# Optimization experiments

Hardware: AMD Instinct MI355X
Metric: run time of the kernel (lower is better)

The kernel has to match this reference:

```python
import jax, jax.numpy as jnp
import numpy as np

EPS = 1e-12  # torch F.normalize eps

def _normalize(v):
    return v / jnp.maximum(jnp.linalg.norm(v, axis=-1, keepdims=True), EPS)

def setup_inputs() -> dict:
    key = jax.random.key(0)
    ks = jax.random.split(key, 8)
    N, K, D = 500000, 32, 3
    positions = jax.random.normal(ks[0], (N, D), dtype=jnp.float32)
    neighbors = jax.random.normal(ks[1], (N, K, D), dtype=jnp.float32)
    # tiny MLP params: Linear(D,5) -> ReLU -> Linear(5,5) -> ReLU -> Linear(5,1)
    s1 = 1.0 / np.sqrt(D)
    s2 = 1.0 / np.sqrt(5)
    W1 = jax.random.uniform(ks[2], (5, D), jnp.float32, -s1, s1)
    b1 = jax.random.uniform(ks[3], (5,), jnp.float32, -s1, s1)
    W2 = jax.random.uniform(ks[4], (5, 5), jnp.float32, -s2, s2)
    b2 = jax.random.uniform(ks[5], (5,), jnp.float32, -s2, s2)
    W3 = jax.random.uniform(ks[6], (1, 5), jnp.float32, -s2, s2)
    b3 = jax.random.uniform(ks[7], (1,), jnp.float32, -s2, s2)
    return {"positions": positions, "neighbors": neighbors,
            "W1": W1, "b1": b1, "W2": W2, "b2": b2, "W3": W3, "b3": b3}

def reference(positions, neighbors, W1, b1, W2, b2, W3, b3):
    # [N,K,D] normalized neighbor difference vectors
    diffs = neighbors - positions[:, None, :]
    nd = _normalize(diffs)
    # tiny MLP producing a scalar weight per neighbor
    h = jax.nn.relu(jnp.einsum('nkd,hd->nkh', nd, W1) + b1)
    h = jax.nn.relu(jnp.einsum('nkh,gh->nkg', h, W2) + b2)
    w = jnp.einsum('nkh,oh->nko', h, W3) + b3  # [N,K,1]
    vel = jnp.sum(nd * w, axis=1)  # [N,D]
    return _normalize(vel)
```

## Files before the change

### kernel.cpp

```cpp
#include <hip/hip_runtime.h>


#define K 32

__global__ __launch_bounds__(256) void velvec_kernel(
    const float* __restrict__ pos,
    const float* __restrict__ nbr,
    const float* __restrict__ W1,
    const float* __restrict__ b1,
    const float* __restrict__ W2,
    const float* __restrict__ b2,
    const float* __restrict__ W3,
    const float* __restrict__ b3,
    float* __restrict__ out,
    int N)
{
    const int lane  = threadIdx.x & (K - 1);
    const int point = (int)((blockIdx.x * blockDim.x + threadIdx.x) >> 5);
    if (point >= N) return;

    float w1[5][3], bb1[5], w2[5][5], bb2[5], w3[5];
#pragma unroll
    for (int h = 0; h < 5; ++h) {
        bb1[h] = b1[h];
        bb2[h] = b2[h];
        w3[h]  = W3[h];
#pragma unroll
        for (int d = 0; d < 3; ++d) w1[h][d] = W1[h * 3 + d];
#pragma unroll
        for (int g = 0; g < 5; ++g) w2[h][g] = W2[h * 5 + g];
    }
    const float bb3 = b3[0];

    const float px = pos[point * 3 + 0];
    const float py = pos[point * 3 + 1];
    const float pz = pos[point * 3 + 2];

    const float* nb = nbr + (size_t)point * (K * 3) + lane * 3;
    float dx = nb[0] - px;
    float dy = nb[1] - py;
    float dz = nb[2] - pz;
    float n2 = dx * dx + dy * dy + dz * dz;
    float inv = (n2 > 1e-24f) ? __builtin_amdgcn_rsqf(n2) : 1e12f;
    dx *= inv; dy *= inv; dz *= inv;

    float h1[5];
#pragma unroll
    for (int h = 0; h < 5; ++h) {
        float a = bb1[h];
        a = fmaf(w1[h][0], dx, a);
        a = fmaf(w1[h][1], dy, a);
        a = fmaf(w1[h][2], dz, a);
        h1[h] = fmaxf(a, 0.0f);
    }
    float h2[5];
#pragma unroll
    for (int g = 0; g < 5; ++g) {
        float a = bb2[g];
#pragma unroll
        for (int h = 0; h < 5; ++h) a = fmaf(w2[g][h], h1[h], a);
        h2[g] = fmaxf(a, 0.0f);
    }
    float w = bb3;
#pragma unroll
    for (int h = 0; h < 5; ++h) w = fmaf(w3[h], h2[h], w);

    float vx = dx * w, vy = dy * w, vz = dz * w;
#pragma unroll
    for (int m = 16; m > 0; m >>= 1) {
        vx += __shfl_xor(vx, m, K);
        vy += __shfl_xor(vy, m, K);
        vz += __shfl_xor(vz, m, K);
    }

    float vn2  = vx * vx + vy * vy + vz * vz;
    float vinv = (vn2 > 1e-24f) ? __builtin_amdgcn_rsqf(vn2) : 1e12f;
    if (lane < 3) {
        float c = (lane == 0) ? vx : (lane == 1) ? vy : vz;
        out[point * 3 + lane] = c * vinv;
    }
}

extern "C" void kernel_launch(void* const* d_in, const int* in_sizes, int n_in,
                              void* d_out, int out_size, void* d_ws, size_t ws_size,
                              hipStream_t stream) {
    const float* pos = (const float*)d_in[0];
    const float* nbr = (const float*)d_in[1];
    const float* W1  = (const float*)d_in[2];
    const float* b1  = (const float*)d_in[3];
    const float* W2  = (const float*)d_in[4];
    const float* b2  = (const float*)d_in[5];
    const float* W3  = (const float*)d_in[6];
    const float* b3  = (const float*)d_in[7];
    float* out = (float*)d_out;

    const int N = in_sizes[0] / 3;
    const int threads = 256;
    const long long total = (long long)N * K;
    const int blocks = (int)((total + threads - 1) / threads);

    velvec_kernel<<<blocks, threads, 0, stream>>>(pos, nbr, W1, b1, W2, b2, W3, b3,
                                                  out, N);
}
```

Baseline: 280.3 us.

## Process four neighbors per thread with vectorized nontemporal loads

Each point now uses 8 threads instead of 32, and each thread handles 4 neighbors. A thread loads its 12 contiguous floats with three 16-byte nontemporal vector loads and accumulates the velocity locally before a shorter 3-step shuffle reduction. This is meant to cut per-neighbor load instructions, redundant per-thread weight and position loads, and shuffle work in a bandwidth-bound kernel. In exchange there are 4x fewer threads, so less parallelism and more serial work per thread.

```diff
diff --git a/kernel.cpp b/kernel.cpp
--- a/kernel.cpp
+++ b/kernel.cpp
@@ -1,7 +1,11 @@
 #include <hip/hip_runtime.h>
 
 
-#define K 32
+#define K   32
+#define LPP 8
+#define NPL 4
+
+typedef float f32x4 __attribute__((ext_vector_type(4)));
 
 __global__ __launch_bounds__(256) void velvec_kernel(
     const float* __restrict__ pos,
@@ -15,16 +19,27 @@
     float* __restrict__ out,
     int N)
 {
-    const int lane  = threadIdx.x & (K - 1);
-    const int point = (int)((blockIdx.x * blockDim.x + threadIdx.x) >> 5);
+    const int tid   = blockIdx.x * blockDim.x + threadIdx.x;
+    const int point = tid >> 3;
+    const int sub   = threadIdx.x & (LPP - 1);
     if (point >= N) return;
 
-    float w1[5][3], bb1[5], w2[5][5], bb2[5], w3[5];
+    const f32x4* nb4 = reinterpret_cast<const f32x4*>(nbr)
+                     + (size_t)point * (K * 3 / 4) + sub * 3;
+    const f32x4 f0 = __builtin_nontemporal_load(nb4 + 0);
+    const f32x4 f1 = __builtin_nontemporal_load(nb4 + 1);
+    const f32x4 f2 = __builtin_nontemporal_load(nb4 + 2);
+
+    const float px = pos[point * 3 + 0];
+    const float py = pos[point * 3 + 1];
+    const float pz = pos[point * 3 + 2];
+
+    float w1[5][3], bb1[5], w2[5][5], bb2[5], w3v[5];
 #pragma unroll
     for (int h = 0; h < 5; ++h) {
         bb1[h] = b1[h];
         bb2[h] = b2[h];
-        w3[h]  = W3[h];
+        w3v[h] = W3[h];
 #pragma unroll
         for (int d = 0; d < 3; ++d) w1[h][d] = W1[h * 3 + d];
 #pragma unroll
@@ -32,52 +47,58 @@
     }
     const float bb3 = b3[0];
 
-    const float px = pos[point * 3 + 0];
-    const float py = pos[point * 3 + 1];
-    const float pz = pos[point * 3 + 2];
+    const float nx[NPL] = { f0.x, f0.w, f1.z, f2.y };
+    const float ny[NPL] = { f0.y, f1.x, f1.w, f2.z };
+    const float nz[NPL] = { f0.z, f1.y, f2.x, f2.w };
 
-    const float* nb = nbr + (size_t)point * (K * 3) + lane * 3;
-    float dx = nb[0] - px;
-    float dy = nb[1] - py;
-    float dz = nb[2] - pz;
-    float n2 = dx * dx + dy * dy + dz * dz;
-    float inv = (n2 > 1e-24f) ? __builtin_amdgcn_rsqf(n2) : 1e12f;
-    dx *= inv; dy *= inv; dz *= inv;
+    float vx = 0.0f, vy = 0.0f, vz = 0.0f;
+#pragma unroll
+    for (int j = 0; j < NPL; ++j) {
+        float dx = nx[j] - px;
+        float dy = ny[j] - py;
+        float dz = nz[j] - pz;
+        float n2 = fmaf(dx, dx, fmaf(dy, dy, dz * dz));
+        float inv = (n2 > 1e-24f) ? __builtin_amdgcn_rsqf(n2) : 1e12f;
+        dx *= inv; dy *= inv; dz *= inv;
 
-    float h1[5];
+        float h1[5];
 #pragma unroll
-    for (int h = 0; h < 5; ++h) {
-        float a = bb1[h];
-        a = fmaf(w1[h][0], dx, a);
-        a = fmaf(w1[h][1], dy, a);
-        a = fmaf(w1[h][2], dz, a);
-        h1[h] = fmaxf(a, 0.0f);
-    }
-    float h2[5];
+        for (int h = 0; h < 5; ++h) {
+            float a = bb1[h];
+            a = fmaf(w1[h][0], dx, a);
+            a = fmaf(w1[h][1], dy, a);
+            a = fmaf(w1[h][2], dz, a);
+            h1[h] = fmaxf(a, 0.0f);
+        }
+        float h2[5];
 #pragma unroll
-    for (int g = 0; g < 5; ++g) {
-        float a = bb2[g];
+        for (int g = 0; g < 5; ++g) {
+            float a = bb2[g];
 #pragma unroll
-        for (int h = 0; h < 5; ++h) a = fmaf(w2[g][h], h1[h], a);
-        h2[g] = fmaxf(a, 0.0f);
-    }
-    float w = bb3;
+            for (int h = 0; h < 5; ++h) a = fmaf(w2[g][h], h1[h], a);
+            h2[g] = fmaxf(a, 0.0f);
+        }
+        float w = bb3;
 #pragma unroll
-    for (int h = 0; h < 5; ++h) w = fmaf(w3[h], h2[h], w);
+        for (int h = 0; h < 5; ++h) w = fmaf(w3v[h], h2[h], w);
 
-    float vx = dx * w, vy = dy * w, vz = dz * w;
-#pragma unroll
-    for (int m = 16; m > 0; m >>= 1) {
-        vx += __shfl_xor(vx, m, K);
-        vy += __shfl_xor(vy, m, K);
-        vz += __shfl_xor(vz, m, K);
+        vx = fmaf(dx, w, vx);
+        vy = fmaf(dy, w, vy);
+        vz = fmaf(dz, w, vz);
     }
 
-    float vn2  = vx * vx + vy * vy + vz * vz;
+#pragma unroll
+    for (int m = LPP / 2; m > 0; m >>= 1) {
+        vx += __shfl_xor(vx, m, LPP);
+        vy += __shfl_xor(vy, m, LPP);
+        vz += __shfl_xor(vz, m, LPP);
+    }
+
+    float vn2  = fmaf(vx, vx, fmaf(vy, vy, vz * vz));
     float vinv = (vn2 > 1e-24f) ? __builtin_amdgcn_rsqf(vn2) : 1e12f;
-    if (lane < 3) {
-        float c = (lane == 0) ? vx : (lane == 1) ? vy : vz;
-        out[point * 3 + lane] = c * vinv;
+    if (sub < 3) {
+        float c = (sub == 0) ? vx : (sub == 1) ? vy : vz;
+        out[point * 3 + sub] = c * vinv;
     }
 }
 
@@ -96,7 +117,7 @@
 
     const int N = in_sizes[0] / 3;
     const int threads = 256;
-    const long long total = (long long)N * K;
+    const long long total = (long long)N * LPP;
     const int blocks = (int)((total + threads - 1) / threads);
 
     velvec_kernel<<<blocks, threads, 0, stream>>>(pos, nbr, W1, b1, W2, b2, W3, b3,
```

New measurement: 281.2 us. About the same (+0.3%).
